# Kernel tuning notes

Measured on AMD Instinct MI355X. Metric: run time of the kernel, lower is better.

Reference implementation:

```python
import jax, jax.numpy as jnp
import numpy as np

NUM_CAMS = 4
E = 256          # embed_dim
H_HEADS = 8      # num_heads
DH = E // H_HEADS
CIN = 64
FF = 4 * E
N_LAYERS = 2
EPS = 1e-5


def _layer_norm(x, g, b):
    mu = jnp.mean(x, axis=-1, keepdims=True)
    var = jnp.mean((x - mu) ** 2, axis=-1, keepdims=True)
    return (x - mu) * jax.lax.rsqrt(var + EPS) * g + b


def setup_inputs() -> dict:
    key = jax.random.key(0)
    ks = jax.random.split(key, 20)
    s = 0.02
    inp = {
        "features": jax.random.normal(ks[0], (NUM_CAMS, 2, CIN, 96, 96), jnp.float32),
        # 1x1 input projection conv
        "Wp": jax.random.normal(ks[1], (E, CIN), jnp.float32) * s,
        "bp": jnp.zeros((E,), jnp.float32),
        # per-layer attention params (stacked over 2 layers)
        "Wqkv": jax.random.normal(ks[2], (N_LAYERS, 3 * E, E), jnp.float32) * s,
        "bqkv": jnp.zeros((N_LAYERS, 3 * E), jnp.float32),
        "Wo": jax.random.normal(ks[3], (N_LAYERS, E, E), jnp.float32) * s,
        "bo": jnp.zeros((N_LAYERS, E), jnp.float32),
        # FFN
        "W1": jax.random.normal(ks[4], (N_LAYERS, FF, E), jnp.float32) * s,
        "b1": jnp.zeros((N_LAYERS, FF), jnp.float32),
        "W2": jax.random.normal(ks[5], (N_LAYERS, E, FF), jnp.float32) * s,
        "b2": jnp.zeros((N_LAYERS, E), jnp.float32),
        # LayerNorms
        "g1": jnp.ones((N_LAYERS, E), jnp.float32),
        "be1": jnp.zeros((N_LAYERS, E), jnp.float32),
        "g2": jnp.ones((N_LAYERS, E), jnp.float32),
        "be2": jnp.zeros((N_LAYERS, E), jnp.float32),
        # 1x1 output conv
        "Wout": jax.random.normal(ks[6], (CIN, E), jnp.float32) * s,
        "bout": jnp.zeros((CIN,), jnp.float32),
    }
    return inp


def reference(features, Wp, bp, Wqkv, bqkv, Wo, bo, W1, b1, W2, b2,
              g1, be1, g2, be2, Wout, bout):
    n_cam, B, Cin, Hh, Ww = features.shape
    # 1x1 conv projection + rearrange to per-pixel sequences: [B*H*W, n_cam, E]
    x = jnp.einsum('nbchw,ec->bhwne', features, Wp) + bp
    x = x.reshape(B * Hh * Ww, n_cam, E)

    scale = 1.0 / jnp.sqrt(jnp.float32(DH))
    for i in range(N_LAYERS):
        # self-attention (post-norm encoder layer, dropout=identity in eval)
        qkv = x @ Wqkv[i].T + bqkv[i]                      # [N, S, 3E]
        q, k, v = jnp.split(qkv, 3, axis=-1)
        q = q.reshape(-1, n_cam, H_HEADS, DH)
        k = k.reshape(-1, n_cam, H_HEADS, DH)
        v = v.reshape(-1, n_cam, H_HEADS, DH)
        scores = jnp.einsum('nqhd,nkhd->nhqk', q, k) * scale
        attn = jax.nn.softmax(scores, axis=-1)
        sa = jnp.einsum('nhqk,nkhd->nqhd', attn, v).reshape(-1, n_cam, E)
        sa = sa @ Wo[i].T + bo[i]
        x = _layer_norm(x + sa, g1[i], be1[i])
        # FFN (ReLU activation, default)
        ff = jax.nn.relu(x @ W1[i].T + b1[i]) @ W2[i].T + b2[i]
        x = _layer_norm(x + ff, g2[i], be2[i])

    # mean over cameras, back to [B, C, H, W] via 1x1 output conv
    fused = x.mean(axis=1).reshape(B, Hh, Ww, E)
    out = jnp.einsum('bhwe,ce->bchw', fused, Wout) + bout[None, :, None, None]
    return out
```

## Files before the change

### kernel.cpp

```cpp
#include <hip/hip_runtime.h>
#include <cstdint>
#include <cstddef>


typedef __bf16 bf16;
typedef __bf16 bf16x8 __attribute__((ext_vector_type(8)));
typedef __bf16 bf16x4 __attribute__((ext_vector_type(4)));
typedef float  f32x4  __attribute__((ext_vector_type(4)));

__device__ __forceinline__ void async_copy16(const void* g, void* l)
{
    __builtin_amdgcn_global_load_lds(
        (__attribute__((address_space(1))) void*)g,
        (__attribute__((address_space(3))) void*)l,
        16, 0, 0);
}

#define WAITV4_BAR() asm volatile("s_waitcnt vmcnt(4)\ns_barrier" ::: "memory")
#define WAITV0_BAR() asm volatile("s_waitcnt vmcnt(0)\ns_barrier" ::: "memory")
#define WAITL_BAR()  asm volatile("s_waitcnt lgkmcnt(0)\ns_barrier" ::: "memory")

__global__ void pack_all_k(const float* __restrict__ s0, const float* __restrict__ s1,
                           const float* __restrict__ s2, const float* __restrict__ s3,
                           const float* __restrict__ s4,
                           bf16* __restrict__ d0, bf16* __restrict__ d1,
                           bf16* __restrict__ d2, bf16* __restrict__ d3,
                           bf16* __restrict__ d4)
{
    const int i = blockIdx.x * 256 + threadIdx.x;
    if (i < 393216)       d0[i] = (bf16)s0[i];
    else if (i < 524288)  d1[i - 393216] = (bf16)s1[i - 393216];
    else if (i < 1048576) d2[i - 524288] = (bf16)s2[i - 524288];
    else if (i < 1572864) d3[i - 1048576] = (bf16)s3[i - 1048576];
    else                  d4[i - 1572864] = (bf16)s4[i - 1572864];
}

__global__ __launch_bounds__(256) void feat_pack_k(const float* __restrict__ feat,
                                                   bf16* __restrict__ Xf)
{
    __shared__ float ft[64][68];

    const int tid  = threadIdx.x;
    const int camb = blockIdx.y;
    const int cam  = camb >> 1;
    const int b    = camb & 1;
    const int hw0  = blockIdx.x * 64;

    const float* fb = feat + (size_t)camb * 64 * 9216 + hw0;
#pragma unroll
    for (int rep = 0; rep < 16; ++rep) {
        const int idx = rep * 256 + tid;
        const int c = idx >> 6, p = idx & 63;
        ft[p][c] = fb[(size_t)c * 9216 + p];
    }
    __syncthreads();

    const int pbase = b * 9216 + hw0;
#pragma unroll
    for (int rep = 0; rep < 2; ++rep) {
        const int idx = rep * 256 + tid;
        const int p = idx >> 3, cc = idx & 7;
        const f32x4 a = *(const f32x4*)(&ft[p][cc * 8]);
        const f32x4 c4 = *(const f32x4*)(&ft[p][cc * 8 + 4]);
        bf16x8 v;
#pragma unroll
        for (int i = 0; i < 4; ++i) { v[i] = (bf16)a[i]; v[4 + i] = (bf16)c4[i]; }
        const size_t t = (size_t)(pbase + p) * 4 + cam;
        *(bf16x8*)(Xf + t * 64 + cc * 8) = v;
    }
}

template <bool RELU>
__global__ __launch_bounds__(256, 2) void gemm_bt(
    const bf16* __restrict__ A, const bf16* __restrict__ B,
    const float* __restrict__ bias, bf16* __restrict__ C,
    int N, int K)
{
    __shared__ __align__(16) bf16 As[128 * 64];
    __shared__ __align__(16) bf16 Bs[128 * 64];

    const int tid  = threadIdx.x;
    const int lane = tid & 63;
    const int wv   = tid >> 6;
    const int wm   = wv >> 1;
    const int wn   = wv & 1;
    const int bm   = blockIdx.y * 128;
    const int bn   = blockIdx.x * 128;

    const int r8  = lane >> 3;
    const int p8  = lane & 7;
    const int gch = p8 ^ r8;

    const int quad = lane >> 4;
    const int l16  = lane & 15;

    f32x4 acc[4][4] = {};

    for (int k0 = 0; k0 < K; k0 += 64) {
#pragma unroll
        for (int inst = 0; inst < 4; ++inst) {
            const int row = wv * 32 + inst * 8 + r8;
            const bf16* ga = A + (size_t)(bm + row) * K + (k0 + gch * 8);
            const bf16* gb = B + (size_t)(bn + row) * K + (k0 + gch * 8);
            async_copy16(ga, (char*)As + (wv * 4 + inst) * 1024);
            async_copy16(gb, (char*)Bs + (wv * 4 + inst) * 1024);
        }
        __syncthreads();

#pragma unroll
        for (int kk = 0; kk < 2; ++kk) {
            bf16x8 af[4], bfr[4];
            const int lch = kk * 4 + quad;
#pragma unroll
            for (int i = 0; i < 4; ++i) {
                const int m = wm * 64 + i * 16 + l16;
                af[i] = *(const bf16x8*)((const char*)As + (m * 8 + (lch ^ (m & 7))) * 16);
                const int n = wn * 64 + i * 16 + l16;
                bfr[i] = *(const bf16x8*)((const char*)Bs + (n * 8 + (lch ^ (n & 7))) * 16);
            }
#pragma unroll
            for (int i = 0; i < 4; ++i)
#pragma unroll
                for (int j = 0; j < 4; ++j)
                    acc[i][j] = __builtin_amdgcn_mfma_f32_16x16x32_bf16(
                        af[i], bfr[j], acc[i][j], 0, 0, 0);
        }
        __syncthreads();
    }

#pragma unroll
    for (int j = 0; j < 4; ++j) {
        const int n = bn + wn * 64 + j * 16 + l16;
        const float bv = bias[n];
#pragma unroll
        for (int i = 0; i < 4; ++i) {
            const int mb = bm + wm * 64 + i * 16 + quad * 4;
#pragma unroll
            for (int r = 0; r < 4; ++r) {
                float v = acc[i][j][r] + bv;
                if (RELU) v = fmaxf(v, 0.f);
                C[(size_t)(mb + r) * N + n] = (bf16)v;
            }
        }
    }
}

__global__ __launch_bounds__(256, 2) void gemm_ln_k(
    const bf16* __restrict__ A, const bf16* __restrict__ B,
    const float* __restrict__ bias, const bf16* __restrict__ Xres,
    const float* __restrict__ gam, const float* __restrict__ bet,
    bf16* __restrict__ Xout, int K)
{
    __shared__ __align__(16) bf16 S[24576];
    __shared__ float2 red[128][2];

    const int tid  = threadIdx.x;
    const int lane = tid & 63;
    const int wv   = tid >> 6;
    const int wm   = wv >> 1;
    const int wn   = wv & 1;
    const int bm   = blockIdx.x * 128;
    const int quad = lane >> 4;
    const int l16  = lane & 15;

    f32x4 acc[4][8] = {};

    for (int k0 = 0; k0 < K; k0 += 64) {
#pragma unroll
        for (int s = 0; s < 12; ++s) {
            const int L   = s * 256 + tid;
            const int row = L >> 3;
            const int gch = (L & 7) ^ (row & 7);
            const bf16* g = (row < 128)
                ? A + (size_t)(bm + row) * K + (k0 + gch * 8)
                : B + (size_t)(row - 128) * K + (k0 + gch * 8);
            async_copy16(g, (char*)S + (size_t)L * 16);
        }
        __syncthreads();

#pragma unroll
        for (int kk = 0; kk < 2; ++kk) {
            const int lch = kk * 4 + quad;
            bf16x8 af[4], bfr[8];
#pragma unroll
            for (int i = 0; i < 4; ++i) {
                const int m = wm * 64 + i * 16 + l16;
                af[i] = *(const bf16x8*)((const char*)S + (m * 8 + (lch ^ (m & 7))) * 16);
            }
#pragma unroll
            for (int j = 0; j < 8; ++j) {
                const int n = wn * 128 + j * 16 + l16;
                bfr[j] = *(const bf16x8*)((const char*)S + ((128 + n) * 8 + (lch ^ (n & 7))) * 16);
            }
#pragma unroll
            for (int i = 0; i < 4; ++i)
#pragma unroll
                for (int j = 0; j < 8; ++j)
                    acc[i][j] = __builtin_amdgcn_mfma_f32_16x16x32_bf16(
                        af[i], bfr[j], acc[i][j], 0, 0, 0);
        }
        __syncthreads();
    }

    float bv[8], gv[8], bev[8];
#pragma unroll
    for (int j = 0; j < 8; ++j) {
        const int n = wn * 128 + j * 16 + l16;
        bv[j] = bias[n]; gv[j] = gam[n]; bev[j] = bet[n];
    }

#pragma unroll
    for (int i = 0; i < 4; ++i) {
#pragma unroll
        for (int r = 0; r < 4; ++r) {
            const int rl  = wm * 64 + i * 16 + quad * 4 + r;
            const size_t row = (size_t)(bm + rl);
            float s1 = 0.f, s2 = 0.f;
#pragma unroll
            for (int j = 0; j < 8; ++j) {
                const int n = wn * 128 + j * 16 + l16;
                const float v = acc[i][j][r] + bv[j] + (float)Xres[row * 256 + n];
                acc[i][j][r] = v;
                s1 += v; s2 += v * v;
            }
#pragma unroll
            for (int off = 1; off < 16; off <<= 1) {
                s1 += __shfl_xor(s1, off, 64);
                s2 += __shfl_xor(s2, off, 64);
            }
            if (l16 == 0) red[rl][wn] = make_float2(s1, s2);
        }
    }
    __syncthreads();

#pragma unroll
    for (int i = 0; i < 4; ++i) {
#pragma unroll
        for (int r = 0; r < 4; ++r) {
            const int rl = wm * 64 + i * 16 + quad * 4 + r;
            const float2 p0 = red[rl][0], p1 = red[rl][1];
            const float mu  = (p0.x + p1.x) * (1.f / 256.f);
            const float ex2 = (p0.y + p1.y) * (1.f / 256.f);
            const float rstd = rsqrtf(fmaxf(ex2 - mu * mu, 0.f) + 1e-5f);
            const size_t row = (size_t)(bm + rl);
#pragma unroll
            for (int j = 0; j < 8; ++j) {
                const int n = wn * 128 + j * 16 + l16;
                Xout[row * 256 + n] = (bf16)((acc[i][j][r] - mu) * rstd * gv[j] + bev[j]);
            }
        }
    }
}

__device__ __forceinline__ void ffn_stage(int s, int rot, const bf16* __restrict__ W1,
                                          const bf16* __restrict__ W2,
                                          char* buf, int tid)
{
    const int hc = ((s >> 3) + rot) & 7;
    const int q  = s & 7;
    if (q < 4) {
#pragma unroll
        for (int it = 0; it < 4; ++it) {
            const int L = it * 256 + tid;
            const int row = L >> 3, psl = L & 7;
            const int c = psl ^ (row & 7);
            async_copy16(W1 + (size_t)(hc * 128 + row) * 256 + q * 64 + c * 8,
                         buf + (size_t)L * 16);
        }
    } else {
#pragma unroll
        for (int it = 0; it < 4; ++it) {
            const int L = it * 256 + tid;
            const int r128 = L >> 3, psl = L & 7;
            const int g = psl ^ (r128 & 7);
            const int n = r128 * 2 + (g >> 2);
            const int c = g & 3;
            async_copy16(W2 + (size_t)n * 1024 + hc * 128 + (q - 4) * 32 + c * 8,
                         buf + (size_t)L * 16);
        }
    }
}

__global__ __launch_bounds__(256, 2) void ffn_fused_k(
    const bf16* __restrict__ X,
    const bf16* __restrict__ W1, const float* __restrict__ b1,
    const bf16* __restrict__ W2, const float* __restrict__ b2,
    const float* __restrict__ gam, const float* __restrict__ bet,
    bf16* __restrict__ Xout)
{
    __shared__ __align__(16) char smem[81920];
    bf16* Xs = (bf16*)smem;
    bf16* Ts = (bf16*)(smem + 32768);
    float2 (*red)[2] = (float2 (*)[2])(void*)(smem + 32768);
    char* stg = smem + 49152;

    const int tid  = threadIdx.x;
    const int lane = tid & 63;
    const int wv   = tid >> 6;
    const int wm   = wv >> 1;
    const int wn   = wv & 1;
    const int quad = lane >> 4;
    const int l16  = lane & 15;
    const int bm   = blockIdx.x * 64;
    const int rot  = (blockIdx.x >> 3) & 7;

#pragma unroll
    for (int it = 0; it < 8; ++it) {
        const int L = it * 256 + tid;
        const int row = L >> 5, slot = L & 31;
        const int gch = (slot & 24) | ((slot ^ row) & 7);
        async_copy16(X + (size_t)(bm + row) * 256 + gch * 8,
                     (char*)Xs + (size_t)L * 16);
    }
    ffn_stage(0, rot, W1, W2, stg, tid);
    ffn_stage(1, rot, W1, W2, stg + 16384, tid);

    f32x4 acc2[2][8] = {};

#pragma unroll 1
    for (int hc = 0; hc < 8; ++hc) {
        const int hcr = (hc + rot) & 7;
        float b1v[4];
#pragma unroll
        for (int j = 0; j < 4; ++j)
            b1v[j] = b1[hcr * 128 + wn * 64 + j * 16 + l16];

        f32x4 accA[2][4] = {};

#pragma unroll
        for (int q = 0; q < 4; ++q) {
            const int s = hc * 8 + q;
            const char* cur = stg + (size_t)(q & 1) * 16384;
            ffn_stage(s + 1, rot, W1, W2, stg + (size_t)((q + 1) & 1) * 16384, tid);
            WAITV4_BAR();
#pragma unroll
            for (int kk = 0; kk < 2; ++kk) {
                const int ch = kk * 4 + quad;
                const int gc = q * 8 + ch;
                bf16x8 af[2], bfr[4];
#pragma unroll
                for (int i = 0; i < 2; ++i) {
                    const int m  = wm * 32 + i * 16 + l16;
                    const int sl = (gc & 24) | ((gc ^ m) & 7);
                    af[i] = *(const bf16x8*)((const char*)Xs + (m * 32 + sl) * 16);
                }
#pragma unroll
                for (int j = 0; j < 4; ++j) {
                    const int n  = wn * 64 + j * 16 + l16;
                    const int sl = ch ^ (n & 7);
                    bfr[j] = *(const bf16x8*)(cur + (n * 8 + sl) * 16);
                }
                __builtin_amdgcn_s_setprio(1);
#pragma unroll
                for (int i = 0; i < 2; ++i)
#pragma unroll
                    for (int j = 0; j < 4; ++j)
                        accA[i][j] = __builtin_amdgcn_mfma_f32_16x16x32_bf16(
                            af[i], bfr[j], accA[i][j], 0, 0, 0);
                __builtin_amdgcn_s_setprio(0);
            }
            WAITL_BAR();
        }

#pragma unroll
        for (int j = 0; j < 4; ++j) {
            const int h  = wn * 64 + j * 16 + l16;
            const float bb = b1v[j];
            const int g  = h >> 3;
#pragma unroll
            for (int i = 0; i < 2; ++i)
#pragma unroll
                for (int r = 0; r < 4; ++r) {
                    const int m  = wm * 32 + i * 16 + quad * 4 + r;
                    const int sl = (g & 8) | ((g ^ m) & 7);
                    const float v = fmaxf(accA[i][j][r] + bb, 0.f);
                    *((bf16*)((char*)Ts + (m * 16 + sl) * 16 + (h & 7) * 2)) = (bf16)v;
                }
        }
        WAITL_BAR();

#pragma unroll
        for (int q = 0; q < 4; ++q) {
            const int s = hc * 8 + 4 + q;
            const char* cur = stg + (size_t)(q & 1) * 16384;
            if (s < 63) {
                ffn_stage(s + 1, rot, W1, W2, stg + (size_t)((q + 1) & 1) * 16384, tid);
                WAITV4_BAR();
            } else {
                WAITV0_BAR();
            }
            const int tc = q * 4 + quad;
            bf16x8 af[2], bfr[8];
#pragma unroll
            for (int i = 0; i < 2; ++i) {
                const int m  = wm * 32 + i * 16 + l16;
                const int sl = (tc & 8) | ((tc ^ m) & 7);
                af[i] = *(const bf16x8*)((const char*)Ts + (m * 16 + sl) * 16);
            }
#pragma unroll
            for (int j = 0; j < 8; ++j) {
                const int n  = wn * 128 + j * 16 + l16;
                const int sl = (((n & 1) * 4 + quad) ^ ((n >> 1) & 7)) & 7;
                bfr[j] = *(const bf16x8*)(cur + ((n >> 1) * 8 + sl) * 16);
            }
            __builtin_amdgcn_s_setprio(1);
#pragma unroll
            for (int i = 0; i < 2; ++i)
#pragma unroll
                for (int j = 0; j < 8; ++j)
                    acc2[i][j] = __builtin_amdgcn_mfma_f32_16x16x32_bf16(
                        af[i], bfr[j], acc2[i][j], 0, 0, 0);
            __builtin_amdgcn_s_setprio(0);
            WAITL_BAR();
        }
    }

    float bv[8], gv[8], bev[8];
#pragma unroll
    for (int j = 0; j < 8; ++j) {
        const int n = wn * 128 + j * 16 + l16;
        bv[j] = b2[n]; gv[j] = gam[n]; bev[j] = bet[n];
    }

#pragma unroll
    for (int i = 0; i < 2; ++i) {
#pragma unroll
        for (int r = 0; r < 4; ++r) {
            const int rl = wm * 32 + i * 16 + quad * 4 + r;
            float s1 = 0.f, s2 = 0.f;
#pragma unroll
            for (int j = 0; j < 8; ++j) {
                const int n  = wn * 128 + j * 16 + l16;
                const int gc = n >> 3;
                const int sl = (gc & 24) | ((gc ^ rl) & 7);
                const float xr = (float)*((const bf16*)((const char*)Xs +
                                   (rl * 32 + sl) * 16 + (n & 7) * 2));
                const float v = acc2[i][j][r] + bv[j] + xr;
                acc2[i][j][r] = v;
                s1 += v; s2 += v * v;
            }
#pragma unroll
            for (int off = 1; off < 16; off <<= 1) {
                s1 += __shfl_xor(s1, off, 64);
                s2 += __shfl_xor(s2, off, 64);
            }
            if (l16 == 0) red[rl][wn] = make_float2(s1, s2);
        }
    }
    __syncthreads();

#pragma unroll
    for (int i = 0; i < 2; ++i) {
#pragma unroll
        for (int r = 0; r < 4; ++r) {
            const int rl = wm * 32 + i * 16 + quad * 4 + r;
            const float2 p0 = red[rl][0], p1 = red[rl][1];
            const float mu  = (p0.x + p1.x) * (1.f / 256.f);
            const float ex2 = (p0.y + p1.y) * (1.f / 256.f);
            const float rstd = rsqrtf(fmaxf(ex2 - mu * mu, 0.f) + 1e-5f);
            const size_t row = (size_t)(bm + rl);
#pragma unroll
            for (int j = 0; j < 8; ++j) {
                const int n = wn * 128 + j * 16 + l16;
                Xout[row * 256 + n] = (bf16)((acc2[i][j][r] - mu) * rstd * gv[j] + bev[j]);
            }
        }
    }
}

__global__ __launch_bounds__(256) void attention_k(const bf16* __restrict__ QKV,
                                                   bf16* __restrict__ SA)
{
    __shared__ float qf[4][4][768];
    __shared__ float sc[4][8][4][4];

    const int tid  = threadIdx.x;
    const int wv   = tid >> 6;
    const int lane = tid & 63;
    const int s    = blockIdx.x * 4 + wv;

    const bf16* base = QKV + (size_t)s * 4 * 768;
#pragma unroll
    for (int it = 0; it < 6; ++it) {
        const int idx = it * 64 + lane;
        const bf16x8 v = *(const bf16x8*)(base + idx * 8);
        const int tok = idx / 96;
        const int e   = (idx % 96) * 8;
        f32x4 f0, f1;
#pragma unroll
        for (int i = 0; i < 4; ++i) { f0[i] = (float)v[i]; f1[i] = (float)v[4 + i]; }
        *(f32x4*)(&qf[wv][tok][e])     = f0;
        *(f32x4*)(&qf[wv][tok][e + 4]) = f1;
    }
    __syncthreads();

#pragma unroll
    for (int rep = 0; rep < 2; ++rep) {
        const int t = rep * 64 + lane;
        const int h = t >> 4, i = (t >> 2) & 3, j = t & 3;
        const float* q = &qf[wv][i][h * 32];
        const float* k = &qf[wv][j][256 + h * 32];
        float a = 0.f;
#pragma unroll
        for (int dd = 0; dd < 32; ++dd) {
            const int d = (dd + lane) & 31;
            a += q[d] * k[d];
        }
        sc[wv][h][i][j] = a * 0.17677669529663687f;
    }
    __syncthreads();

    if (lane < 32) {
        const int h = lane >> 2, i = lane & 3;
        float s0 = sc[wv][h][i][0], s1 = sc[wv][h][i][1];
        float s2 = sc[wv][h][i][2], s3 = sc[wv][h][i][3];
        float m = fmaxf(fmaxf(s0, s1), fmaxf(s2, s3));
        float e0 = expf(s0 - m), e1 = expf(s1 - m);
        float e2 = expf(s2 - m), e3 = expf(s3 - m);
        float inv = 1.f / (e0 + e1 + e2 + e3);
        sc[wv][h][i][0] = e0 * inv;
        sc[wv][h][i][1] = e1 * inv;
        sc[wv][h][i][2] = e2 * inv;
        sc[wv][h][i][3] = e3 * inv;
    }
    __syncthreads();

    const int h = lane >> 3;
#pragma unroll
    for (int i = 0; i < 4; ++i) {
        f32x4 a = {0.f, 0.f, 0.f, 0.f};
#pragma unroll
        for (int j = 0; j < 4; ++j) {
            const float p = sc[wv][h][i][j];
            const f32x4 v = *(const f32x4*)(&qf[wv][j][512 + lane * 4]);
#pragma unroll
            for (int q = 0; q < 4; ++q) a[q] += p * v[q];
        }
        bf16x4 o;
#pragma unroll
        for (int q = 0; q < 4; ++q) o[q] = (bf16)a[q];
        *(bf16x4*)(SA + (size_t)(s * 4 + i) * 256 + lane * 4) = o;
    }
}

__global__ __launch_bounds__(256) void out_proj_k(const bf16* __restrict__ X,
                                                  const float* __restrict__ Wout,
                                                  const float* __restrict__ bout,
                                                  float* __restrict__ out)
{
    __shared__ float fused[16][260];
    const int tid = threadIdx.x;
    const int p0  = blockIdx.x * 16;

#pragma unroll
    for (int it = 0; it < 16; ++it) {
        const int idx = it * 256 + tid;
        const int pix = idx >> 8, e = idx & 255;
        const size_t base = (size_t)(p0 + pix) * 1024 + e;
        const float s = (float)X[base] + (float)X[base + 256] +
                        (float)X[base + 512] + (float)X[base + 768];
        fused[pix][e] = s * 0.25f;
    }
    __syncthreads();

    const int pix = tid & 15;
    const int c0  = tid >> 4;
    const int p   = p0 + pix;
    const int b   = p / 9216;
    const int hw  = p % 9216;
#pragma unroll
    for (int it = 0; it < 4; ++it) {
        const int c = it * 16 + c0;
        const float* w = Wout + c * 256;
        float acc = bout[c];
#pragma unroll 8
        for (int e = 0; e < 256; ++e) acc += fused[pix][e] * w[e];
        out[((size_t)b * 64 + c) * 9216 + hw] = acc;
    }
}

extern "C" void kernel_launch(void* const* d_in, const int* in_sizes, int n_in,
                              void* d_out, int out_size, void* d_ws, size_t ws_size,
                              hipStream_t stream)
{
    const float* features = (const float*)d_in[0];
    const float* Wp   = (const float*)d_in[1];
    const float* bp   = (const float*)d_in[2];
    const float* Wqkv = (const float*)d_in[3];
    const float* bqkv = (const float*)d_in[4];
    const float* Wo   = (const float*)d_in[5];
    const float* bo   = (const float*)d_in[6];
    const float* W1   = (const float*)d_in[7];
    const float* b1   = (const float*)d_in[8];
    const float* W2   = (const float*)d_in[9];
    const float* b2   = (const float*)d_in[10];
    const float* g1   = (const float*)d_in[11];
    const float* be1  = (const float*)d_in[12];
    const float* g2   = (const float*)d_in[13];
    const float* be2  = (const float*)d_in[14];
    const float* Wout = (const float*)d_in[15];
    const float* bout = (const float*)d_in[16];
    float* out = (float*)d_out;

    char* ws = (char*)d_ws;
    bf16* X   = (bf16*)(ws);
    bf16* QKV = (bf16*)(ws + 37748736ull);
    bf16* SAb = (bf16*)(ws + 150994944ull);
    bf16* Xf  = (bf16*)(ws + 188743680ull);
    bf16* WpB = (bf16*)(ws + 198180864ull);
    bf16* Wb  = (bf16*)(ws + 226492416ull);

    bf16* WqkvB = Wb;
    bf16* WoB   = Wb + 393216;
    bf16* W1B   = Wb + 524288;
    bf16* W2B   = Wb + 1048576;

    pack_all_k<<<6208, 256, 0, stream>>>(Wqkv, Wo, W1, W2, Wp,
                                         WqkvB, WoB, W1B, W2B, WpB);

    feat_pack_k<<<dim3(144, 8), 256, 0, stream>>>(features, Xf);
    gemm_bt<false><<<dim3(2, 576), 256, 0, stream>>>(Xf, WpB, bp, X, 256, 64);

    for (int l = 0; l < 2; ++l) {
        gemm_bt<false><<<dim3(6, 576), 256, 0, stream>>>(
            X, WqkvB + l * 196608, bqkv + l * 768, QKV, 768, 256);
        attention_k<<<4608, 256, 0, stream>>>(QKV, SAb);
        gemm_ln_k<<<576, 256, 0, stream>>>(
            SAb, WoB + l * 65536, bo + l * 256, X,
            g1 + l * 256, be1 + l * 256, X, 256);
        ffn_fused_k<<<1152, 256, 0, stream>>>(
            X, W1B + l * 262144, b1 + l * 1024,
            W2B + l * 262144, b2 + l * 256,
            g2 + l * 256, be2 + l * 256, X);
    }

    out_proj_k<<<1152, 256, 0, stream>>>(X, Wout, bout, out);
}
```

Before: 660.0 us.

## Fuse per-pixel attention into the Wo projection + LayerNorm kernel

Attention for the block's 32 pixel sequences (128 rows) is computed inside the output-projection/LayerNorm kernel and written directly into a swizzled LDS tile, which then serves as the GEMM A operand. This removes the separate attention kernel and the global round trip of the SA tensor. Each wave prefetches the next sequence's QKV into registers while computing the current one. The kernel now uses about 132 KB of LDS, limiting occupancy to one block per CU, and the attention phase runs serially with no overlap with the GEMM.

```diff
diff --git a/kernel.cpp b/kernel.cpp
--- a/kernel.cpp
+++ b/kernel.cpp
@@ -19,6 +19,7 @@
 #define WAITV4_BAR() asm volatile("s_waitcnt vmcnt(4)\ns_barrier" ::: "memory")
 #define WAITV0_BAR() asm volatile("s_waitcnt vmcnt(0)\ns_barrier" ::: "memory")
 #define WAITL_BAR()  asm volatile("s_waitcnt lgkmcnt(0)\ns_barrier" ::: "memory")
+#define WAITL()      asm volatile("s_waitcnt lgkmcnt(0)" ::: "memory")
 
 __global__ void pack_all_k(const float* __restrict__ s0, const float* __restrict__ s1,
                            const float* __restrict__ s2, const float* __restrict__ s3,
@@ -145,52 +146,152 @@
     }
 }
 
-__global__ __launch_bounds__(256, 2) void gemm_ln_k(
-    const bf16* __restrict__ A, const bf16* __restrict__ B,
+__global__ __launch_bounds__(256) void attn_ln_k(
+    const bf16* __restrict__ QKV, const bf16* __restrict__ B,
     const float* __restrict__ bias, const bf16* __restrict__ Xres,
     const float* __restrict__ gam, const float* __restrict__ bet,
-    bf16* __restrict__ Xout, int K)
-{
-    __shared__ __align__(16) bf16 S[24576];
-    __shared__ float2 red[128][2];
+    bf16* __restrict__ Xout)
+{
+    __shared__ __align__(16) char smem[135168];
+    bf16*  SAs  = (bf16*)smem;
+    char*  Bbuf = smem + 65536;
+    float* qf   = (float*)(smem + 65536);
+    float* sc   = (float*)(smem + 131072);
+    float2 (*red)[2] = (float2 (*)[2])(void*)(smem + 133120);
 
     const int tid  = threadIdx.x;
     const int lane = tid & 63;
     const int wv   = tid >> 6;
     const int wm   = wv >> 1;
     const int wn   = wv & 1;
-    const int bm   = blockIdx.x * 128;
     const int quad = lane >> 4;
     const int l16  = lane & 15;
+    const int bm   = blockIdx.x * 128;
+
+    float* qf_w = qf + wv * 3072;
+    float* sc_w = sc + wv * 128;
+
+    {
+        const int s0 = blockIdx.x * 32;
+        bf16x8 nv[6];
+        {
+            const bf16* bse = QKV + (size_t)(s0 + wv) * 3072;
+#pragma unroll
+            for (int it = 0; it < 6; ++it)
+                nv[it] = *(const bf16x8*)(bse + (it * 64 + lane) * 8);
+        }
+#pragma unroll
+        for (int g = 0; g < 8; ++g) {
+#pragma unroll
+            for (int it = 0; it < 6; ++it) {
+                const int idx = it * 64 + lane;
+                const int tok = idx / 96;
+                const int e   = (idx % 96) * 8;
+                f32x4 f0, f1;
+#pragma unroll
+                for (int i = 0; i < 4; ++i) {
+                    f0[i] = (float)nv[it][i]; f1[i] = (float)nv[it][4 + i];
+                }
+                *(f32x4*)(qf_w + tok * 768 + e)     = f0;
+                *(f32x4*)(qf_w + tok * 768 + e + 4) = f1;
+            }
+            bf16x8 nx[6];
+            if (g < 7) {
+                const bf16* bse = QKV + (size_t)(s0 + (g + 1) * 4 + wv) * 3072;
+#pragma unroll
+                for (int it = 0; it < 6; ++it)
+                    nx[it] = *(const bf16x8*)(bse + (it * 64 + lane) * 8);
+            }
+            WAITL();
+
+#pragma unroll
+            for (int rep = 0; rep < 2; ++rep) {
+                const int t = rep * 64 + lane;
+                const int h = t >> 4, i = (t >> 2) & 3, j = t & 3;
+                const float* q = qf_w + i * 768 + h * 32;
+                const float* k = qf_w + j * 768 + 256 + h * 32;
+                float a = 0.f;
+#pragma unroll
+                for (int dd = 0; dd < 32; ++dd) {
+                    const int d = (dd + lane) & 31;
+                    a += q[d] * k[d];
+                }
+                sc_w[h * 16 + i * 4 + j] = a * 0.17677669529663687f;
+            }
+            WAITL();
+
+            if (lane < 32) {
+                const int h = lane >> 2, i = lane & 3;
+                float v0 = sc_w[h * 16 + i * 4 + 0];
+                float v1 = sc_w[h * 16 + i * 4 + 1];
+                float v2 = sc_w[h * 16 + i * 4 + 2];
+                float v3 = sc_w[h * 16 + i * 4 + 3];
+                const float m = fmaxf(fmaxf(v0, v1), fmaxf(v2, v3));
+                const float e0 = expf(v0 - m), e1 = expf(v1 - m);
+                const float e2 = expf(v2 - m), e3 = expf(v3 - m);
+                const float inv = 1.f / (e0 + e1 + e2 + e3);
+                sc_w[h * 16 + i * 4 + 0] = e0 * inv;
+                sc_w[h * 16 + i * 4 + 1] = e1 * inv;
+                sc_w[h * 16 + i * 4 + 2] = e2 * inv;
+                sc_w[h * 16 + i * 4 + 3] = e3 * inv;
+            }
+            WAITL();
+
+            const int h = lane >> 3;
+#pragma unroll
+            for (int i = 0; i < 4; ++i) {
+                f32x4 a = {0.f, 0.f, 0.f, 0.f};
+#pragma unroll
+                for (int j = 0; j < 4; ++j) {
+                    const float p = sc_w[h * 16 + i * 4 + j];
+                    const f32x4 v = *(const f32x4*)(qf_w + j * 768 + 512 + lane * 4);
+#pragma unroll
+                    for (int q = 0; q < 4; ++q) a[q] += p * v[q];
+                }
+                bf16x4 o;
+#pragma unroll
+                for (int q = 0; q < 4; ++q) o[q] = (bf16)a[q];
+                const int m  = (g * 4 + wv) * 4 + i;
+                const int gc = lane >> 1;
+                const int sl = (gc & 24) | ((gc ^ m) & 7);
+                *(bf16x4*)((char*)SAs + (m * 32 + sl) * 16 + (lane & 1) * 8) = o;
+            }
+#pragma unroll
+            for (int it = 0; it < 6; ++it) nv[it] = nx[it];
+        }
+    }
+    __syncthreads();
 
     f32x4 acc[4][8] = {};
 
-    for (int k0 = 0; k0 < K; k0 += 64) {
-#pragma unroll
-        for (int s = 0; s < 12; ++s) {
-            const int L   = s * 256 + tid;
+#pragma unroll 1
+    for (int c0 = 0; c0 < 4; ++c0) {
+        char* buf = Bbuf + (size_t)(c0 & 1) * 32768;
+#pragma unroll
+        for (int it = 0; it < 8; ++it) {
+            const int L   = it * 256 + tid;
             const int row = L >> 3;
             const int gch = (L & 7) ^ (row & 7);
-            const bf16* g = (row < 128)
-                ? A + (size_t)(bm + row) * K + (k0 + gch * 8)
-                : B + (size_t)(row - 128) * K + (k0 + gch * 8);
-            async_copy16(g, (char*)S + (size_t)L * 16);
+            async_copy16(B + (size_t)row * 256 + (c0 * 64 + gch * 8),
+                         buf + (size_t)L * 16);
         }
         __syncthreads();
 
 #pragma unroll
         for (int kk = 0; kk < 2; ++kk) {
             const int lch = kk * 4 + quad;
+            const int gc  = c0 * 8 + lch;
             bf16x8 af[4], bfr[8];
 #pragma unroll
             for (int i = 0; i < 4; ++i) {
-                const int m = wm * 64 + i * 16 + l16;
-                af[i] = *(const bf16x8*)((const char*)S + (m * 8 + (lch ^ (m & 7))) * 16);
+                const int m  = wm * 64 + i * 16 + l16;
+                const int sl = (gc & 24) | ((gc ^ m) & 7);
+                af[i] = *(const bf16x8*)((const char*)SAs + (m * 32 + sl) * 16);
             }
 #pragma unroll
             for (int j = 0; j < 8; ++j) {
                 const int n = wn * 128 + j * 16 + l16;
-                bfr[j] = *(const bf16x8*)((const char*)S + ((128 + n) * 8 + (lch ^ (n & 7))) * 16);
+                bfr[j] = *(const bf16x8*)(buf + (n * 8 + (lch ^ (n & 7))) * 16);
             }
 #pragma unroll
             for (int i = 0; i < 4; ++i)
@@ -465,81 +566,6 @@
                 Xout[row * 256 + n] = (bf16)((acc2[i][j][r] - mu) * rstd * gv[j] + bev[j]);
             }
         }
-    }
-}
-
-__global__ __launch_bounds__(256) void attention_k(const bf16* __restrict__ QKV,
-                                                   bf16* __restrict__ SA)
-{
-    __shared__ float qf[4][4][768];
-    __shared__ float sc[4][8][4][4];
-
-    const int tid  = threadIdx.x;
-    const int wv   = tid >> 6;
-    const int lane = tid & 63;
-    const int s    = blockIdx.x * 4 + wv;
-
-    const bf16* base = QKV + (size_t)s * 4 * 768;
-#pragma unroll
-    for (int it = 0; it < 6; ++it) {
-        const int idx = it * 64 + lane;
-        const bf16x8 v = *(const bf16x8*)(base + idx * 8);
-        const int tok = idx / 96;
-        const int e   = (idx % 96) * 8;
-        f32x4 f0, f1;
-#pragma unroll
-        for (int i = 0; i < 4; ++i) { f0[i] = (float)v[i]; f1[i] = (float)v[4 + i]; }
-        *(f32x4*)(&qf[wv][tok][e])     = f0;
-        *(f32x4*)(&qf[wv][tok][e + 4]) = f1;
-    }
-    __syncthreads();
-
-#pragma unroll
-    for (int rep = 0; rep < 2; ++rep) {
-        const int t = rep * 64 + lane;
-        const int h = t >> 4, i = (t >> 2) & 3, j = t & 3;
-        const float* q = &qf[wv][i][h * 32];
-        const float* k = &qf[wv][j][256 + h * 32];
-        float a = 0.f;
-#pragma unroll
-        for (int dd = 0; dd < 32; ++dd) {
-            const int d = (dd + lane) & 31;
-            a += q[d] * k[d];
-        }
-        sc[wv][h][i][j] = a * 0.17677669529663687f;
-    }
-    __syncthreads();
-
-    if (lane < 32) {
-        const int h = lane >> 2, i = lane & 3;
-        float s0 = sc[wv][h][i][0], s1 = sc[wv][h][i][1];
-        float s2 = sc[wv][h][i][2], s3 = sc[wv][h][i][3];
-        float m = fmaxf(fmaxf(s0, s1), fmaxf(s2, s3));
-        float e0 = expf(s0 - m), e1 = expf(s1 - m);
-        float e2 = expf(s2 - m), e3 = expf(s3 - m);
-        float inv = 1.f / (e0 + e1 + e2 + e3);
-        sc[wv][h][i][0] = e0 * inv;
-        sc[wv][h][i][1] = e1 * inv;
-        sc[wv][h][i][2] = e2 * inv;
-        sc[wv][h][i][3] = e3 * inv;
-    }
-    __syncthreads();
-
-    const int h = lane >> 3;
-#pragma unroll
-    for (int i = 0; i < 4; ++i) {
-        f32x4 a = {0.f, 0.f, 0.f, 0.f};
-#pragma unroll
-        for (int j = 0; j < 4; ++j) {
-            const float p = sc[wv][h][i][j];
-            const f32x4 v = *(const f32x4*)(&qf[wv][j][512 + lane * 4]);
-#pragma unroll
-            for (int q = 0; q < 4; ++q) a[q] += p * v[q];
-        }
-        bf16x4 o;
-#pragma unroll
-        for (int q = 0; q < 4; ++q) o[q] = (bf16)a[q];
-        *(bf16x4*)(SA + (size_t)(s * 4 + i) * 256 + lane * 4) = o;
     }
 }
 
@@ -605,7 +631,6 @@
     char* ws = (char*)d_ws;
     bf16* X   = (bf16*)(ws);
     bf16* QKV = (bf16*)(ws + 37748736ull);
-    bf16* SAb = (bf16*)(ws + 150994944ull);
     bf16* Xf  = (bf16*)(ws + 188743680ull);
     bf16* WpB = (bf16*)(ws + 198180864ull);
     bf16* Wb  = (bf16*)(ws + 226492416ull);
@@ -624,10 +649,9 @@
     for (int l = 0; l < 2; ++l) {
         gemm_bt<false><<<dim3(6, 576), 256, 0, stream>>>(
             X, WqkvB + l * 196608, bqkv + l * 768, QKV, 768, 256);
-        attention_k<<<4608, 256, 0, stream>>>(QKV, SAb);
-        gemm_ln_k<<<576, 256, 0, stream>>>(
-            SAb, WoB + l * 65536, bo + l * 256, X,
-            g1 + l * 256, be1 + l * 256, X, 256);
+        attn_ln_k<<<576, 256, 0, stream>>>(
+            QKV, WoB + l * 65536, bo + l * 256, X,
+            g1 + l * 256, be1 + l * 256, X);
         ffn_fused_k<<<1152, 256, 0, stream>>>(
             X, W1B + l * 262144, b1 + l * 1024,
             W2B + l * 262144, b2 + l * 256,
```

New measurement: 727.7 us. 10.3% more time.
